# Kernel tuning notes

Measured on AMD Instinct MI355X. Metric: run time of the kernel, lower is better.

The kernel has to match this reference:

```python
import jax, jax.numpy as jnp
import numpy as np

B, T, D, E, F = 4, 2048, 1024, 8, 1024

def setup_inputs() -> dict:
    key = jax.random.key(0)
    ks = jax.random.split(key, 5)
    s = lambda d: 1.0 / np.sqrt(d)
    return {
        "x": jax.random.normal(ks[0], (B, T, D), dtype=jnp.float32),
        "router_kernel_DE": jax.random.normal(ks[1], (D, E), dtype=jnp.float32) * s(D),
        "kernel_gating_EDF": jax.random.normal(ks[2], (E, D, F), dtype=jnp.float32) * s(D),
        "kernel_up_EDF": jax.random.normal(ks[3], (E, D, F), dtype=jnp.float32) * s(D),
        "kernel_down_EFD": jax.random.normal(ks[4], (E, F, D), dtype=jnp.float32) * s(F),
        "top_k": 2,
    }

def reference(x, router_kernel_DE, kernel_gating_EDF, kernel_up_EDF, kernel_down_EFD, top_k):
    # ---- Router ----
    router_logits_BTE = jnp.einsum('BTD,DE->BTE', x, router_kernel_DE)
    probs_BTE = jax.nn.softmax(router_logits_BTE.astype(jnp.float32), axis=-1)
    weights_BTX, selected_BTX = jax.lax.top_k(probs_BTE, top_k)
    # module re-normalizes top-k weights with a second softmax (faithful)
    norm_weights_BTX = jax.nn.softmax(weights_BTX, axis=-1)
    # ---- combine weights to dense per-expert weights ----
    one_hot_BTXE = jax.nn.one_hot(selected_BTX, num_classes=E, dtype=jnp.float32)
    full_weights_BTE = jnp.sum(one_hot_BTXE * norm_weights_BTX[..., None], axis=2)
    # ---- dense all-experts MLP (apply_expert_weight_before_computation=False) ----
    gating_BTEF = jnp.einsum('BTD,EDF->BTEF', x, kernel_gating_EDF)
    up_BTEF = jnp.einsum('BTD,EDF->BTEF', x, kernel_up_EDF)
    fuse_BTEF = jax.nn.silu(gating_BTEF) * up_BTEF
    down_BTED = jnp.einsum('BTEF,EFD->BTED', fuse_BTEF, kernel_down_EFD)
    out_BTD = jnp.einsum('BTED,BTE->BTD', down_BTED, full_weights_BTE)
    return out_BTD
```

## Files before the change

### kernel.cpp

```cpp
#include <hip/hip_runtime.h>
#include <hip/hip_bf16.h>
#include <math.h>

#define NTOK 8192
#define D_DIM 1024
#define E_DIM 8
#define F_DIM 1024

#define CNT_STRIDE 32

typedef __attribute__((ext_vector_type(8))) short bf16x8;
typedef __attribute__((ext_vector_type(4))) float f32x4;

typedef const __attribute__((address_space(1))) unsigned int* as1_uint_ptr;
typedef __attribute__((address_space(3))) unsigned int* as3_uint_ptr;

__device__ __forceinline__ void async_load16(const void* g, void* l) {
    __builtin_amdgcn_global_load_lds((as1_uint_ptr)g, (as3_uint_ptr)l, 16, 0, 0);
}

__device__ __forceinline__ float bf2f(unsigned short b) {
    unsigned int u = ((unsigned int)b) << 16;
    return __builtin_bit_cast(float, u);
}
__device__ __forceinline__ unsigned short f2bf(float f) {
    __hip_bfloat16 h = __float2bfloat16(f);
    return __builtin_bit_cast(unsigned short, h);
}


__global__ __launch_bounds__(512) void router_cast_kernel(
    const float* __restrict__ x,
    const float* __restrict__ Wr,
    int* __restrict__ cnt,
    int* __restrict__ tok_of,
    float* __restrict__ wt2,
    unsigned short* __restrict__ xb)
{
    __shared__ int lcnt[E_DIM];
    __shared__ int lbase[E_DIM];
    __shared__ int lbuf[E_DIM][64];

    const int tid = threadIdx.x;
    const int wv = tid >> 6;
    const int lane = tid & 63;
    if (tid < E_DIM) lcnt[tid] = 0;
    __syncthreads();

    #pragma unroll
    for (int it = 0; it < 4; ++it) {
        const int t = blockIdx.x * 32 + wv * 4 + it;
        const float* xrow = x + (size_t)t * D_DIM;
        unsigned short* xbrow = xb + (size_t)t * D_DIM;

        float p[E_DIM];
        #pragma unroll
        for (int e = 0; e < E_DIM; ++e) p[e] = 0.f;

        #pragma unroll
        for (int i = 0; i < 4; ++i) {
            const int d = i * 256 + lane * 4;
            float4 v = *(const float4*)(xrow + d);
            ushort4 o;
            o.x = f2bf(v.x); o.y = f2bf(v.y); o.z = f2bf(v.z); o.w = f2bf(v.w);
            *(ushort4*)(xbrow + d) = o;
            const float* wr = Wr + (size_t)d * E_DIM;
            float xv[4] = {v.x, v.y, v.z, v.w};
            #pragma unroll
            for (int q = 0; q < 4; ++q) {
                float4 w0 = *(const float4*)(wr + q * 8);
                float4 w1 = *(const float4*)(wr + q * 8 + 4);
                p[0] += xv[q] * w0.x; p[1] += xv[q] * w0.y;
                p[2] += xv[q] * w0.z; p[3] += xv[q] * w0.w;
                p[4] += xv[q] * w1.x; p[5] += xv[q] * w1.y;
                p[6] += xv[q] * w1.z; p[7] += xv[q] * w1.w;
            }
        }

        #pragma unroll
        for (int off = 32; off > 0; off >>= 1) {
            #pragma unroll
            for (int e = 0; e < E_DIM; ++e)
                p[e] += __shfl_xor(p[e], off, 64);
        }

        if (lane == 0) {
            float m = p[0];
            #pragma unroll
            for (int e = 1; e < E_DIM; ++e) m = fmaxf(m, p[e]);
            float pr[E_DIM], sum = 0.f;
            #pragma unroll
            for (int e = 0; e < E_DIM; ++e) { pr[e] = expf(p[e] - m); sum += pr[e]; }
            float inv = 1.f / sum;
            #pragma unroll
            for (int e = 0; e < E_DIM; ++e) pr[e] *= inv;
            int e0 = 0;
            #pragma unroll
            for (int e = 1; e < E_DIM; ++e) if (pr[e] > pr[e0]) e0 = e;
            int e1 = (e0 == 0) ? 1 : 0;
            #pragma unroll
            for (int e = 0; e < E_DIM; ++e) { if (e != e0 && pr[e] > pr[e1]) e1 = e; }
            float b = expf(pr[e1] - pr[e0]);
            float w0 = 1.f / (1.f + b);
            float w1 = b / (1.f + b);
            int p0 = atomicAdd(&lcnt[e0], 1);
            lbuf[e0][p0] = t * 2 + 0;
            int p1 = atomicAdd(&lcnt[e1], 1);
            lbuf[e1][p1] = t * 2 + 1;
            wt2[t * 2 + 0] = w0;
            wt2[t * 2 + 1] = w1;
        }
    }
    __syncthreads();
    if (tid < E_DIM) lbase[tid] = atomicAdd(&cnt[tid * CNT_STRIDE], lcnt[tid]);
    __syncthreads();
    #pragma unroll
    for (int e = 0; e < E_DIM; ++e) {
        int n = lcnt[e];
        if (tid < n) tok_of[e * NTOK + lbase[e] + tid] = lbuf[e][tid];
    }
}

__global__ __launch_bounds__(256) void transpose_cast_kernel(
    const float* __restrict__ Wg, const float* __restrict__ Wu,
    const float* __restrict__ Wd,
    unsigned short* __restrict__ WgT, unsigned short* __restrict__ WuT,
    unsigned short* __restrict__ WdT)
{
    const int m = blockIdx.z;
    const float* src;
    unsigned short* dst;
    if (m < 8)       { src = Wg + (size_t)m * 1048576;        dst = WgT + (size_t)m * 1048576; }
    else if (m < 16) { src = Wu + (size_t)(m - 8) * 1048576;  dst = WuT + (size_t)(m - 8) * 1048576; }
    else             { src = Wd + (size_t)(m - 16) * 1048576; dst = WdT + (size_t)(m - 16) * 1048576; }

    const int c0 = blockIdx.x * 64;
    const int r0 = blockIdx.y * 64;
    __shared__ float tile[64][65];
    const int tid = threadIdx.x;
    const int tr = tid >> 4;
    const int tc = (tid & 15) * 4;
    #pragma unroll
    for (int p = 0; p < 4; ++p) {
        float4 v = *(const float4*)(src + (size_t)(r0 + p * 16 + tr) * 1024 + c0 + tc);
        tile[p * 16 + tr][tc + 0] = v.x;
        tile[p * 16 + tr][tc + 1] = v.y;
        tile[p * 16 + tr][tc + 2] = v.z;
        tile[p * 16 + tr][tc + 3] = v.w;
    }
    __syncthreads();
    const int orow = tid >> 3;
    const int ocol = (tid & 7) * 8;
    #pragma unroll
    for (int p = 0; p < 2; ++p) {
        int fr = p * 32 + orow;
        union { unsigned short s[8]; uint4 v; } pk;
        #pragma unroll
        for (int q = 0; q < 8; ++q) pk.s[q] = f2bf(tile[ocol + q][fr]);
        *(uint4*)&dst[(size_t)(c0 + fr) * 1024 + r0 + ocol] = pk.v;
    }
}

__global__ __launch_bounds__(256, 2) void gateup_mfma(
    const unsigned short* __restrict__ xb,
    const unsigned short* __restrict__ WgT,
    const unsigned short* __restrict__ WuT,
    const int* __restrict__ cnt,
    const int* __restrict__ tok_of,
    unsigned short* __restrict__ H)
{
    const int e = blockIdx.y;
    const int rowTile = blockIdx.x >> 3;
    const int colTile = blockIdx.x & 7;
    const int rows = cnt[e * CNT_STRIDE];
    const int rowBase = rowTile * 128;
    if (rowBase >= rows) return;
    const int n0 = colTile * 128;

    __shared__ short As[2][128 * 32];
    __shared__ short Bg[2][128 * 32];
    __shared__ short Bu[2][128 * 32];
    __shared__ int toks[128];

    const int tid = threadIdx.x;
    if (tid < 128) {
        int idx = rowBase + tid;
        toks[tid] = tok_of[e * NTOK + (idx < rows ? idx : rows - 1)];
    }
    __syncthreads();

    const int lane = tid & 63;
    const int w = tid >> 6;
    const int seg0 = w * 2, seg1 = w * 2 + 1;
    const int sr = lane >> 2;
    const int swz = (sr >> 1) & 3;
    const int sk = ((lane & 3) ^ swz) * 8;

    const int ar0 = seg0 * 16 + sr;
    const int ar1 = seg1 * 16 + sr;
    const unsigned short* aG0 = xb + (size_t)(toks[ar0] >> 1) * D_DIM + sk;
    const unsigned short* aG1 = xb + (size_t)(toks[ar1] >> 1) * D_DIM + sk;
    const unsigned short* WgTe = WgT + (size_t)e * F_DIM * D_DIM;
    const unsigned short* WuTe = WuT + (size_t)e * F_DIM * D_DIM;
    const unsigned short* gG0 = WgTe + (size_t)(n0 + ar0) * D_DIM + sk;
    const unsigned short* gG1 = WgTe + (size_t)(n0 + ar1) * D_DIM + sk;
    const unsigned short* uG0 = WuTe + (size_t)(n0 + ar0) * D_DIM + sk;
    const unsigned short* uG1 = WuTe + (size_t)(n0 + ar1) * D_DIM + sk;

    const int mseg = (w >> 1) * 4;
    const int nseg = (w & 1) * 4;
    const int mbase = (w >> 1) * 64;
    const int nbase = (w & 1) * 64;
    const int fr = lane & 15;
    const int rd = (4 * fr + ((lane >> 4) ^ ((fr >> 1) & 3))) * 8;

    f32x4 accg[4][4], accu[4][4];
    #pragma unroll
    for (int i = 0; i < 4; ++i)
        #pragma unroll
        for (int j = 0; j < 4; ++j) { accg[i][j] = (f32x4)(0.f); accu[i][j] = (f32x4)(0.f); }

    #define STAGE_GU(b, kk) do { \
        async_load16(aG0 + (kk), &As[b][seg0 * 512]); \
        async_load16(aG1 + (kk), &As[b][seg1 * 512]); \
        async_load16(gG0 + (kk), &Bg[b][seg0 * 512]); \
        async_load16(gG1 + (kk), &Bg[b][seg1 * 512]); \
        async_load16(uG0 + (kk), &Bu[b][seg0 * 512]); \
        async_load16(uG1 + (kk), &Bu[b][seg1 * 512]); \
    } while (0)

    const int NT = D_DIM / 32;
    STAGE_GU(0, 0);
    STAGE_GU(1, 32);

    #pragma unroll 2
    for (int t = 0; t < NT - 1; ++t) {
        const int b = t & 1;
        asm volatile("s_waitcnt vmcnt(6)" ::: "memory");
        __builtin_amdgcn_s_barrier();

        bf16x8 a[4], g[4], u[4];
        #pragma unroll
        for (int i = 0; i < 4; ++i)
            a[i] = *(const bf16x8*)&As[b][(mseg + i) * 512 + rd];
        #pragma unroll
        for (int j = 0; j < 4; ++j) {
            g[j] = *(const bf16x8*)&Bg[b][(nseg + j) * 512 + rd];
            u[j] = *(const bf16x8*)&Bu[b][(nseg + j) * 512 + rd];
        }
        asm volatile("s_waitcnt lgkmcnt(0)" ::: "memory");
        __builtin_amdgcn_sched_barrier(0);
        __builtin_amdgcn_s_barrier();
        if (t < NT - 2) STAGE_GU(b, (t + 2) * 32);

        __builtin_amdgcn_s_setprio(1);
        #pragma unroll
        for (int i = 0; i < 4; ++i)
            #pragma unroll
            for (int j = 0; j < 4; ++j) {
                accg[i][j] = __builtin_amdgcn_mfma_f32_16x16x32_bf16(a[i], g[j], accg[i][j], 0, 0, 0);
                accu[i][j] = __builtin_amdgcn_mfma_f32_16x16x32_bf16(a[i], u[j], accu[i][j], 0, 0, 0);
            }
        __builtin_amdgcn_s_setprio(0);
    }
    {
        asm volatile("s_waitcnt vmcnt(0)" ::: "memory");
        __builtin_amdgcn_s_barrier();
        bf16x8 a[4], g[4], u[4];
        #pragma unroll
        for (int i = 0; i < 4; ++i)
            a[i] = *(const bf16x8*)&As[1][(mseg + i) * 512 + rd];
        #pragma unroll
        for (int j = 0; j < 4; ++j) {
            g[j] = *(const bf16x8*)&Bg[1][(nseg + j) * 512 + rd];
            u[j] = *(const bf16x8*)&Bu[1][(nseg + j) * 512 + rd];
        }
        __builtin_amdgcn_s_setprio(1);
        #pragma unroll
        for (int i = 0; i < 4; ++i)
            #pragma unroll
            for (int j = 0; j < 4; ++j) {
                accg[i][j] = __builtin_amdgcn_mfma_f32_16x16x32_bf16(a[i], g[j], accg[i][j], 0, 0, 0);
                accu[i][j] = __builtin_amdgcn_mfma_f32_16x16x32_bf16(a[i], u[j], accu[i][j], 0, 0, 0);
            }
        __builtin_amdgcn_s_setprio(0);
    }
    #undef STAGE_GU

    const int erow = (lane >> 4) * 4;
    #pragma unroll
    for (int i = 0; i < 4; ++i) {
        #pragma unroll
        for (int r = 0; r < 4; ++r) {
            int row = mbase + i * 16 + erow + r;
            int idx = rowBase + row;
            if (idx < rows) {
                int tok2 = toks[row];
                unsigned short* hrow = H + (size_t)tok2 * F_DIM + n0 + nbase;
                #pragma unroll
                for (int j = 0; j < 4; ++j) {
                    float gg = accg[i][j][r];
                    float uu = accu[i][j][r];
                    float h = gg / (1.f + __expf(-gg)) * uu;
                    hrow[j * 16 + fr] = f2bf(h);
                }
            }
        }
    }
}

__global__ __launch_bounds__(256, 2) void down_mfma(
    const unsigned short* __restrict__ H,
    const unsigned short* __restrict__ WdT,
    const int* __restrict__ cnt,
    const int* __restrict__ tok_of,
    unsigned short* __restrict__ Hd)
{
    const int e = blockIdx.y;
    const int rowTile = blockIdx.x >> 3;
    const int colTile = blockIdx.x & 7;
    const int rows = cnt[e * CNT_STRIDE];
    const int rowBase = rowTile * 128;
    if (rowBase >= rows) return;
    const int n0 = colTile * 128;

    __shared__ short As[2][128 * 32];
    __shared__ short Bs[2][128 * 32];
    __shared__ int toks[128];

    const int tid = threadIdx.x;
    if (tid < 128) {
        int idx = rowBase + tid;
        toks[tid] = tok_of[e * NTOK + (idx < rows ? idx : rows - 1)];
    }
    __syncthreads();

    const int lane = tid & 63;
    const int w = tid >> 6;
    const int seg0 = w * 2, seg1 = w * 2 + 1;
    const int sr = lane >> 2;
    const int swz = (sr >> 1) & 3;
    const int sk = ((lane & 3) ^ swz) * 8;

    const int ar0 = seg0 * 16 + sr;
    const int ar1 = seg1 * 16 + sr;
    const unsigned short* aG0 = H + (size_t)toks[ar0] * F_DIM + sk;
    const unsigned short* aG1 = H + (size_t)toks[ar1] * F_DIM + sk;
    const unsigned short* WdTe = WdT + (size_t)e * D_DIM * F_DIM;
    const unsigned short* bG0 = WdTe + (size_t)(n0 + ar0) * F_DIM + sk;
    const unsigned short* bG1 = WdTe + (size_t)(n0 + ar1) * F_DIM + sk;

    const int mseg = (w >> 1) * 4;
    const int nseg = (w & 1) * 4;
    const int mbase = (w >> 1) * 64;
    const int nbase = (w & 1) * 64;
    const int fr = lane & 15;
    const int rd = (4 * fr + ((lane >> 4) ^ ((fr >> 1) & 3))) * 8;

    f32x4 acc[4][4];
    #pragma unroll
    for (int i = 0; i < 4; ++i)
        #pragma unroll
        for (int j = 0; j < 4; ++j) acc[i][j] = (f32x4)(0.f);

    #define STAGE_D(b, kk) do { \
        async_load16(aG0 + (kk), &As[b][seg0 * 512]); \
        async_load16(aG1 + (kk), &As[b][seg1 * 512]); \
        async_load16(bG0 + (kk), &Bs[b][seg0 * 512]); \
        async_load16(bG1 + (kk), &Bs[b][seg1 * 512]); \
    } while (0)

    const int NT = F_DIM / 32;
    STAGE_D(0, 0);
    STAGE_D(1, 32);

    #pragma unroll 2
    for (int t = 0; t < NT - 1; ++t) {
        const int b = t & 1;
        asm volatile("s_waitcnt vmcnt(4)" ::: "memory");
        __builtin_amdgcn_s_barrier();

        bf16x8 a[4], bb[4];
        #pragma unroll
        for (int i = 0; i < 4; ++i)
            a[i] = *(const bf16x8*)&As[b][(mseg + i) * 512 + rd];
        #pragma unroll
        for (int j = 0; j < 4; ++j)
            bb[j] = *(const bf16x8*)&Bs[b][(nseg + j) * 512 + rd];

        asm volatile("s_waitcnt lgkmcnt(0)" ::: "memory");
        __builtin_amdgcn_sched_barrier(0);
        __builtin_amdgcn_s_barrier();
        if (t < NT - 2) STAGE_D(b, (t + 2) * 32);

        __builtin_amdgcn_s_setprio(1);
        #pragma unroll
        for (int i = 0; i < 4; ++i)
            #pragma unroll
            for (int j = 0; j < 4; ++j)
                acc[i][j] = __builtin_amdgcn_mfma_f32_16x16x32_bf16(a[i], bb[j], acc[i][j], 0, 0, 0);
        __builtin_amdgcn_s_setprio(0);
    }
    {
        asm volatile("s_waitcnt vmcnt(0)" ::: "memory");
        __builtin_amdgcn_s_barrier();
        bf16x8 a[4], bb[4];
        #pragma unroll
        for (int i = 0; i < 4; ++i)
            a[i] = *(const bf16x8*)&As[1][(mseg + i) * 512 + rd];
        #pragma unroll
        for (int j = 0; j < 4; ++j)
            bb[j] = *(const bf16x8*)&Bs[1][(nseg + j) * 512 + rd];
        __builtin_amdgcn_s_setprio(1);
        #pragma unroll
        for (int i = 0; i < 4; ++i)
            #pragma unroll
            for (int j = 0; j < 4; ++j)
                acc[i][j] = __builtin_amdgcn_mfma_f32_16x16x32_bf16(a[i], bb[j], acc[i][j], 0, 0, 0);
        __builtin_amdgcn_s_setprio(0);
    }
    #undef STAGE_D

    const int erow = (lane >> 4) * 4;
    #pragma unroll
    for (int i = 0; i < 4; ++i) {
        #pragma unroll
        for (int r = 0; r < 4; ++r) {
            int row = mbase + i * 16 + erow + r;
            int idx = rowBase + row;
            if (idx < rows) {
                int tok2 = toks[row];
                unsigned short* orow = Hd + (size_t)tok2 * D_DIM + n0 + nbase;
                #pragma unroll
                for (int j = 0; j < 4; ++j)
                    orow[j * 16 + fr] = f2bf(acc[i][j][r]);
            }
        }
    }
}

__global__ __launch_bounds__(256) void combine_kernel(
    const unsigned short* __restrict__ Hd,
    const float* __restrict__ wt2,
    float* __restrict__ out)
{
    const int t = blockIdx.x;
    const int tid = threadIdx.x;
    const float w0 = wt2[2 * t];
    const float w1 = wt2[2 * t + 1];
    const int c = tid * 4;
    ushort4 a = *(const ushort4*)&Hd[(size_t)(2 * t) * D_DIM + c];
    ushort4 b = *(const ushort4*)&Hd[(size_t)(2 * t + 1) * D_DIM + c];
    float4 o;
    o.x = w0 * bf2f(a.x) + w1 * bf2f(b.x);
    o.y = w0 * bf2f(a.y) + w1 * bf2f(b.y);
    o.z = w0 * bf2f(a.z) + w1 * bf2f(b.z);
    o.w = w0 * bf2f(a.w) + w1 * bf2f(b.w);
    *(float4*)(out + (size_t)t * D_DIM + c) = o;
}

extern "C" void kernel_launch(void* const* d_in, const int* in_sizes, int n_in,
                              void* d_out, int out_size, void* d_ws, size_t ws_size,
                              hipStream_t stream) {
    const float* x  = (const float*)d_in[0];
    const float* Wr = (const float*)d_in[1];
    const float* Wg = (const float*)d_in[2];
    const float* Wu = (const float*)d_in[3];
    const float* Wd = (const float*)d_in[4];
    float* out = (float*)d_out;

    char* ws = (char*)d_ws;
    int*   cnt    = (int*)ws;
    int*   tok_of = (int*)(ws + 1024);
    float* wt2    = (float*)(ws + 1024 + E_DIM * NTOK * 4);
    char*  base   = ws + (1 << 20);
    unsigned short* xb  = (unsigned short*)(base);
    unsigned short* Hd  = (unsigned short*)(base);
    unsigned short* WgT = (unsigned short*)(base + (16ll << 20));
    unsigned short* WuT = (unsigned short*)(base + (32ll << 20));
    unsigned short* WdT = (unsigned short*)(base + (48ll << 20));
    unsigned short* H   = (unsigned short*)(base + (64ll << 20));

    hipMemsetAsync(cnt, 0, E_DIM * CNT_STRIDE * sizeof(int), stream);

    router_cast_kernel<<<NTOK / 32, 512, 0, stream>>>(x, Wr, cnt, tok_of, wt2, xb);
    transpose_cast_kernel<<<dim3(16, 16, 24), 256, 0, stream>>>(Wg, Wu, Wd, WgT, WuT, WdT);

    gateup_mfma<<<dim3((NTOK / 128) * (F_DIM / 128), E_DIM), 256, 0, stream>>>(
        xb, WgT, WuT, cnt, tok_of, H);
    down_mfma<<<dim3((NTOK / 128) * (D_DIM / 128), E_DIM), 256, 0, stream>>>(
        H, WdT, cnt, tok_of, Hd);
    combine_kernel<<<NTOK, 256, 0, stream>>>(Hd, wt2, out);
}
```

Before: 361.4 us.

## Triple-buffer LDS pipelines and use 256-row tiles in down projection

Both the gate/up and down GEMM kernels move from double to triple-buffered LDS staging. The next-next tile is now issued right after a single barrier at the top of each iteration, removing the second barrier per k-step. The down kernel's M tile also doubles to 256 rows, with each wave computing 8x4 MFMA fragments and a correspondingly smaller grid, to raise B-operand reuse. In exchange, LDS use and accumulator register pressure go up, which may lower occupancy, and the larger tiles leave more padding waste for partially filled experts.

```diff
diff --git a/kernel.cpp b/kernel.cpp
--- a/kernel.cpp
+++ b/kernel.cpp
@@ -177,9 +177,9 @@
     if (rowBase >= rows) return;
     const int n0 = colTile * 128;
 
-    __shared__ short As[2][128 * 32];
-    __shared__ short Bg[2][128 * 32];
-    __shared__ short Bu[2][128 * 32];
+    __shared__ short As[3][128 * 32];
+    __shared__ short Bg[3][128 * 32];
+    __shared__ short Bu[3][128 * 32];
     __shared__ int toks[128];
 
     const int tid = threadIdx.x;
@@ -207,6 +207,9 @@
     const unsigned short* uG0 = WuTe + (size_t)(n0 + ar0) * D_DIM + sk;
     const unsigned short* uG1 = WuTe + (size_t)(n0 + ar1) * D_DIM + sk;
 
+    const int soff0 = seg0 * 512;
+    const int soff1 = seg1 * 512;
+
     const int mseg = (w >> 1) * 4;
     const int nseg = (w & 1) * 4;
     const int mbase = (w >> 1) * 64;
@@ -220,39 +223,41 @@
         #pragma unroll
         for (int j = 0; j < 4; ++j) { accg[i][j] = (f32x4)(0.f); accu[i][j] = (f32x4)(0.f); }
 
-    #define STAGE_GU(b, kk) do { \
-        async_load16(aG0 + (kk), &As[b][seg0 * 512]); \
-        async_load16(aG1 + (kk), &As[b][seg1 * 512]); \
-        async_load16(gG0 + (kk), &Bg[b][seg0 * 512]); \
-        async_load16(gG1 + (kk), &Bg[b][seg1 * 512]); \
-        async_load16(uG0 + (kk), &Bu[b][seg0 * 512]); \
-        async_load16(uG1 + (kk), &Bu[b][seg1 * 512]); \
+    #define STAGE_GU(bs, kk) do { \
+        async_load16(aG0 + (kk), &As[bs][soff0]); \
+        async_load16(aG1 + (kk), &As[bs][soff1]); \
+        async_load16(gG0 + (kk), &Bg[bs][soff0]); \
+        async_load16(gG1 + (kk), &Bg[bs][soff1]); \
+        async_load16(uG0 + (kk), &Bu[bs][soff0]); \
+        async_load16(uG1 + (kk), &Bu[bs][soff1]); \
     } while (0)
 
     const int NT = D_DIM / 32;
     STAGE_GU(0, 0);
     STAGE_GU(1, 32);
 
-    #pragma unroll 2
+    int bc = 0;
     for (int t = 0; t < NT - 1; ++t) {
-        const int b = t & 1;
+        asm volatile("s_waitcnt lgkmcnt(0)" ::: "memory");
         asm volatile("s_waitcnt vmcnt(6)" ::: "memory");
         __builtin_amdgcn_s_barrier();
-
+        __builtin_amdgcn_sched_barrier(0);
+        if (t + 2 < NT) {
+            int bs = bc + 2; if (bs >= 3) bs -= 3;
+            STAGE_GU(bs, (t + 2) * 32);
+        }
+        const short* Ab = As[bc];
+        const short* Gb = Bg[bc];
+        const short* Ub = Bu[bc];
         bf16x8 a[4], g[4], u[4];
         #pragma unroll
         for (int i = 0; i < 4; ++i)
-            a[i] = *(const bf16x8*)&As[b][(mseg + i) * 512 + rd];
+            a[i] = *(const bf16x8*)&Ab[(mseg + i) * 512 + rd];
         #pragma unroll
         for (int j = 0; j < 4; ++j) {
-            g[j] = *(const bf16x8*)&Bg[b][(nseg + j) * 512 + rd];
-            u[j] = *(const bf16x8*)&Bu[b][(nseg + j) * 512 + rd];
-        }
-        asm volatile("s_waitcnt lgkmcnt(0)" ::: "memory");
-        __builtin_amdgcn_sched_barrier(0);
-        __builtin_amdgcn_s_barrier();
-        if (t < NT - 2) STAGE_GU(b, (t + 2) * 32);
-
+            g[j] = *(const bf16x8*)&Gb[(nseg + j) * 512 + rd];
+            u[j] = *(const bf16x8*)&Ub[(nseg + j) * 512 + rd];
+        }
         __builtin_amdgcn_s_setprio(1);
         #pragma unroll
         for (int i = 0; i < 4; ++i)
@@ -262,18 +267,24 @@
                 accu[i][j] = __builtin_amdgcn_mfma_f32_16x16x32_bf16(a[i], u[j], accu[i][j], 0, 0, 0);
             }
         __builtin_amdgcn_s_setprio(0);
+        if (++bc == 3) bc = 0;
     }
     {
+        asm volatile("s_waitcnt lgkmcnt(0)" ::: "memory");
         asm volatile("s_waitcnt vmcnt(0)" ::: "memory");
         __builtin_amdgcn_s_barrier();
+        __builtin_amdgcn_sched_barrier(0);
+        const short* Ab = As[bc];
+        const short* Gb = Bg[bc];
+        const short* Ub = Bu[bc];
         bf16x8 a[4], g[4], u[4];
         #pragma unroll
         for (int i = 0; i < 4; ++i)
-            a[i] = *(const bf16x8*)&As[1][(mseg + i) * 512 + rd];
+            a[i] = *(const bf16x8*)&Ab[(mseg + i) * 512 + rd];
         #pragma unroll
         for (int j = 0; j < 4; ++j) {
-            g[j] = *(const bf16x8*)&Bg[1][(nseg + j) * 512 + rd];
-            u[j] = *(const bf16x8*)&Bu[1][(nseg + j) * 512 + rd];
+            g[j] = *(const bf16x8*)&Gb[(nseg + j) * 512 + rd];
+            u[j] = *(const bf16x8*)&Ub[(nseg + j) * 512 + rd];
         }
         __builtin_amdgcn_s_setprio(1);
         #pragma unroll
@@ -320,16 +331,16 @@
     const int rowTile = blockIdx.x >> 3;
     const int colTile = blockIdx.x & 7;
     const int rows = cnt[e * CNT_STRIDE];
-    const int rowBase = rowTile * 128;
+    const int rowBase = rowTile * 256;
     if (rowBase >= rows) return;
     const int n0 = colTile * 128;
 
-    __shared__ short As[2][128 * 32];
-    __shared__ short Bs[2][128 * 32];
-    __shared__ int toks[128];
+    __shared__ short As[3][256 * 32];
+    __shared__ short Bs[3][128 * 32];
+    __shared__ int toks[256];
 
     const int tid = threadIdx.x;
-    if (tid < 128) {
+    {
         int idx = rowBase + tid;
         toks[tid] = tok_of[e * NTOK + (idx < rows ? idx : rows - 1)];
     }
@@ -337,93 +348,104 @@
 
     const int lane = tid & 63;
     const int w = tid >> 6;
-    const int seg0 = w * 2, seg1 = w * 2 + 1;
     const int sr = lane >> 2;
     const int swz = (sr >> 1) & 3;
     const int sk = ((lane & 3) ^ swz) * 8;
 
-    const int ar0 = seg0 * 16 + sr;
-    const int ar1 = seg1 * 16 + sr;
-    const unsigned short* aG0 = H + (size_t)toks[ar0] * F_DIM + sk;
-    const unsigned short* aG1 = H + (size_t)toks[ar1] * F_DIM + sk;
+    const int as0 = w * 4, as1 = w * 4 + 1, as2 = w * 4 + 2, as3 = w * 4 + 3;
+    const unsigned short* aG0 = H + (size_t)toks[as0 * 16 + sr] * F_DIM + sk;
+    const unsigned short* aG1 = H + (size_t)toks[as1 * 16 + sr] * F_DIM + sk;
+    const unsigned short* aG2 = H + (size_t)toks[as2 * 16 + sr] * F_DIM + sk;
+    const unsigned short* aG3 = H + (size_t)toks[as3 * 16 + sr] * F_DIM + sk;
+    const int bs0 = w * 2, bs1 = w * 2 + 1;
     const unsigned short* WdTe = WdT + (size_t)e * D_DIM * F_DIM;
-    const unsigned short* bG0 = WdTe + (size_t)(n0 + ar0) * F_DIM + sk;
-    const unsigned short* bG1 = WdTe + (size_t)(n0 + ar1) * F_DIM + sk;
-
-    const int mseg = (w >> 1) * 4;
+    const unsigned short* bG0 = WdTe + (size_t)(n0 + bs0 * 16 + sr) * F_DIM + sk;
+    const unsigned short* bG1 = WdTe + (size_t)(n0 + bs1 * 16 + sr) * F_DIM + sk;
+
+    const int aoff0 = as0 * 512, aoff1 = as1 * 512, aoff2 = as2 * 512, aoff3 = as3 * 512;
+    const int boff0 = bs0 * 512, boff1 = bs1 * 512;
+
+    const int mseg = (w >> 1) * 8;
     const int nseg = (w & 1) * 4;
-    const int mbase = (w >> 1) * 64;
+    const int mbase = (w >> 1) * 128;
     const int nbase = (w & 1) * 64;
     const int fr = lane & 15;
     const int rd = (4 * fr + ((lane >> 4) ^ ((fr >> 1) & 3))) * 8;
 
-    f32x4 acc[4][4];
-    #pragma unroll
-    for (int i = 0; i < 4; ++i)
+    f32x4 acc[8][4];
+    #pragma unroll
+    for (int i = 0; i < 8; ++i)
         #pragma unroll
         for (int j = 0; j < 4; ++j) acc[i][j] = (f32x4)(0.f);
 
-    #define STAGE_D(b, kk) do { \
-        async_load16(aG0 + (kk), &As[b][seg0 * 512]); \
-        async_load16(aG1 + (kk), &As[b][seg1 * 512]); \
-        async_load16(bG0 + (kk), &Bs[b][seg0 * 512]); \
-        async_load16(bG1 + (kk), &Bs[b][seg1 * 512]); \
+    #define STAGE_D(bs, kk) do { \
+        async_load16(aG0 + (kk), &As[bs][aoff0]); \
+        async_load16(aG1 + (kk), &As[bs][aoff1]); \
+        async_load16(aG2 + (kk), &As[bs][aoff2]); \
+        async_load16(aG3 + (kk), &As[bs][aoff3]); \
+        async_load16(bG0 + (kk), &Bs[bs][boff0]); \
+        async_load16(bG1 + (kk), &Bs[bs][boff1]); \
     } while (0)
 
     const int NT = F_DIM / 32;
     STAGE_D(0, 0);
     STAGE_D(1, 32);
 
-    #pragma unroll 2
+    int bc = 0;
     for (int t = 0; t < NT - 1; ++t) {
-        const int b = t & 1;
-        asm volatile("s_waitcnt vmcnt(4)" ::: "memory");
+        asm volatile("s_waitcnt lgkmcnt(0)" ::: "memory");
+        asm volatile("s_waitcnt vmcnt(6)" ::: "memory");
         __builtin_amdgcn_s_barrier();
-
-        bf16x8 a[4], bb[4];
-        #pragma unroll
-        for (int i = 0; i < 4; ++i)
-            a[i] = *(const bf16x8*)&As[b][(mseg + i) * 512 + rd];
+        __builtin_amdgcn_sched_barrier(0);
+        if (t + 2 < NT) {
+            int bs = bc + 2; if (bs >= 3) bs -= 3;
+            STAGE_D(bs, (t + 2) * 32);
+        }
+        const short* Ab = As[bc];
+        const short* Bb = Bs[bc];
+        bf16x8 a[8], b[4];
+        #pragma unroll
+        for (int i = 0; i < 8; ++i)
+            a[i] = *(const bf16x8*)&Ab[(mseg + i) * 512 + rd];
         #pragma unroll
         for (int j = 0; j < 4; ++j)
-            bb[j] = *(const bf16x8*)&Bs[b][(nseg + j) * 512 + rd];
-
+            b[j] = *(const bf16x8*)&Bb[(nseg + j) * 512 + rd];
+        __builtin_amdgcn_s_setprio(1);
+        #pragma unroll
+        for (int i = 0; i < 8; ++i)
+            #pragma unroll
+            for (int j = 0; j < 4; ++j)
+                acc[i][j] = __builtin_amdgcn_mfma_f32_16x16x32_bf16(a[i], b[j], acc[i][j], 0, 0, 0);
+        __builtin_amdgcn_s_setprio(0);
+        if (++bc == 3) bc = 0;
+    }
+    {
         asm volatile("s_waitcnt lgkmcnt(0)" ::: "memory");
-        __builtin_amdgcn_sched_barrier(0);
-        __builtin_amdgcn_s_barrier();
-        if (t < NT - 2) STAGE_D(b, (t + 2) * 32);
-
-        __builtin_amdgcn_s_setprio(1);
-        #pragma unroll
-        for (int i = 0; i < 4; ++i)
-            #pragma unroll
-            for (int j = 0; j < 4; ++j)
-                acc[i][j] = __builtin_amdgcn_mfma_f32_16x16x32_bf16(a[i], bb[j], acc[i][j], 0, 0, 0);
-        __builtin_amdgcn_s_setprio(0);
-    }
-    {
         asm volatile("s_waitcnt vmcnt(0)" ::: "memory");
         __builtin_amdgcn_s_barrier();
-        bf16x8 a[4], bb[4];
-        #pragma unroll
-        for (int i = 0; i < 4; ++i)
-            a[i] = *(const bf16x8*)&As[1][(mseg + i) * 512 + rd];
+        __builtin_amdgcn_sched_barrier(0);
+        const short* Ab = As[bc];
+        const short* Bb = Bs[bc];
+        bf16x8 a[8], b[4];
+        #pragma unroll
+        for (int i = 0; i < 8; ++i)
+            a[i] = *(const bf16x8*)&Ab[(mseg + i) * 512 + rd];
         #pragma unroll
         for (int j = 0; j < 4; ++j)
-            bb[j] = *(const bf16x8*)&Bs[1][(nseg + j) * 512 + rd];
+            b[j] = *(const bf16x8*)&Bb[(nseg + j) * 512 + rd];
         __builtin_amdgcn_s_setprio(1);
         #pragma unroll
-        for (int i = 0; i < 4; ++i)
+        for (int i = 0; i < 8; ++i)
             #pragma unroll
             for (int j = 0; j < 4; ++j)
-                acc[i][j] = __builtin_amdgcn_mfma_f32_16x16x32_bf16(a[i], bb[j], acc[i][j], 0, 0, 0);
+                acc[i][j] = __builtin_amdgcn_mfma_f32_16x16x32_bf16(a[i], b[j], acc[i][j], 0, 0, 0);
         __builtin_amdgcn_s_setprio(0);
     }
     #undef STAGE_D
 
     const int erow = (lane >> 4) * 4;
     #pragma unroll
-    for (int i = 0; i < 4; ++i) {
+    for (int i = 0; i < 8; ++i) {
         #pragma unroll
         for (int r = 0; r < 4; ++r) {
             int row = mbase + i * 16 + erow + r;
@@ -488,7 +510,7 @@
 
     gateup_mfma<<<dim3((NTOK / 128) * (F_DIM / 128), E_DIM), 256, 0, stream>>>(
         xb, WgT, WuT, cnt, tok_of, H);
-    down_mfma<<<dim3((NTOK / 128) * (D_DIM / 128), E_DIM), 256, 0, stream>>>(
+    down_mfma<<<dim3(32 * (D_DIM / 128), E_DIM), 256, 0, stream>>>(
         H, WdT, cnt, tok_of, Hd);
     combine_kernel<<<NTOK, 256, 0, stream>>>(Hd, wt2, out);
 }
```

Result: slower. 383.5 us (+6.1%).

## Compact grouped-GEMM grid to only valid expert row tiles, raise occupancy hint

Applied to the files above, without the earlier changes.

Replaces the fixed per-expert 2D grid, where most blocks exited immediately because each expert only has a fraction of the 8192 tokens, with a flat 1D grid sized to the maximum number of valid tiles. Each block scans the expert counts to find which expert and row tile it owns. This removes the cost of launching and retiring many empty blocks. It also raises the launch-bounds occupancy hint from 2 to 3 blocks per SM, which may push register use down and cause spills.

```diff
diff --git a/kernel.cpp b/kernel.cpp
--- a/kernel.cpp
+++ b/kernel.cpp
@@ -161,7 +161,7 @@
     }
 }
 
-__global__ __launch_bounds__(256, 2) void gateup_mfma(
+__global__ __launch_bounds__(256, 3) void gateup_mfma(
     const unsigned short* __restrict__ xb,
     const unsigned short* __restrict__ WgT,
     const unsigned short* __restrict__ WuT,
@@ -169,12 +169,17 @@
     const int* __restrict__ tok_of,
     unsigned short* __restrict__ H)
 {
-    const int e = blockIdx.y;
-    const int rowTile = blockIdx.x >> 3;
     const int colTile = blockIdx.x & 7;
-    const int rows = cnt[e * CNT_STRIDE];
-    const int rowBase = rowTile * 128;
-    if (rowBase >= rows) return;
+    const int wk = blockIdx.x >> 3;
+    int e = -1, rowBase = 0, rows = 0, tb = 0;
+    #pragma unroll
+    for (int q = 0; q < E_DIM; ++q) {
+        int r = cnt[q * CNT_STRIDE];
+        int nt = (r + 127) >> 7;
+        if (e < 0 && wk < tb + nt) { e = q; rowBase = (wk - tb) << 7; rows = r; }
+        tb += nt;
+    }
+    if (e < 0) return;
     const int n0 = colTile * 128;
 
     __shared__ short As[2][128 * 32];
@@ -309,19 +314,24 @@
     }
 }
 
-__global__ __launch_bounds__(256, 2) void down_mfma(
+__global__ __launch_bounds__(256, 3) void down_mfma(
     const unsigned short* __restrict__ H,
     const unsigned short* __restrict__ WdT,
     const int* __restrict__ cnt,
     const int* __restrict__ tok_of,
     unsigned short* __restrict__ Hd)
 {
-    const int e = blockIdx.y;
-    const int rowTile = blockIdx.x >> 3;
     const int colTile = blockIdx.x & 7;
-    const int rows = cnt[e * CNT_STRIDE];
-    const int rowBase = rowTile * 128;
-    if (rowBase >= rows) return;
+    const int wk = blockIdx.x >> 3;
+    int e = -1, rowBase = 0, rows = 0, tb = 0;
+    #pragma unroll
+    for (int q = 0; q < E_DIM; ++q) {
+        int r = cnt[q * CNT_STRIDE];
+        int nt = (r + 127) >> 7;
+        if (e < 0 && wk < tb + nt) { e = q; rowBase = (wk - tb) << 7; rows = r; }
+        tb += nt;
+    }
+    if (e < 0) return;
     const int n0 = colTile * 128;
 
     __shared__ short As[2][128 * 32];
@@ -486,9 +496,10 @@
     router_cast_kernel<<<NTOK / 32, 512, 0, stream>>>(x, Wr, cnt, tok_of, wt2, xb);
     transpose_cast_kernel<<<dim3(16, 16, 24), 256, 0, stream>>>(Wg, Wu, Wd, WgT, WuT, WdT);
 
-    gateup_mfma<<<dim3((NTOK / 128) * (F_DIM / 128), E_DIM), 256, 0, stream>>>(
+    const int MAX_TILES = (2 * NTOK) / 128 + E_DIM;
+    gateup_mfma<<<dim3(MAX_TILES * 8), 256, 0, stream>>>(
         xb, WgT, WuT, cnt, tok_of, H);
-    down_mfma<<<dim3((NTOK / 128) * (D_DIM / 128), E_DIM), 256, 0, stream>>>(
+    down_mfma<<<dim3(MAX_TILES * 8), 256, 0, stream>>>(
         H, WdT, cnt, tok_of, Hd);
     combine_kernel<<<NTOK, 256, 0, stream>>>(Hd, wt2, out);
 }
```

Result: slower. 654.3 us (+81.0%).
